# Optimization experiments

Hardware: AMD Instinct MI355X
Metric: run time of the kernel (lower is better)

The kernel has to match this reference:

```python
import jax, jax.numpy as jnp
import numpy as np

VOCAB = 100000
DIM = 128
B = 16384
CWIN = 10
K = 10
EPS = 1e-9


def setup_inputs() -> dict:
    key = jax.random.key(0)
    k1, k2, k3, k4, k5 = jax.random.split(key, 5)
    context = jax.random.randint(k1, (B, CWIN), 0, VOCAB)
    target = jax.random.randint(k2, (B,), 0, VOCAB)
    negatives = jax.random.randint(k3, (B, K), 0, VOCAB)
    in_emb = jax.random.normal(k4, (VOCAB, DIM), dtype=jnp.float32)
    out_emb = jax.random.normal(k5, (VOCAB, DIM), dtype=jnp.float32)
    return {"context": context, "target": target, "negatives": negatives,
            "in_emb": in_emb, "out_emb": out_emb}


def reference(context, target, negatives, in_emb, out_emb):
    # context: [B, C] int; target: [B] int; negatives: [B, K] int
    context_embed = in_emb[context]                      # [B, C, D]
    context_mean = jnp.mean(context_embed, axis=1)       # [B, D]
    target_embed = out_emb[target]                       # [B, D]
    neg_embed = out_emb[negatives]                       # [B, K, D]
    pos_score = jnp.sum(context_mean * target_embed, axis=1)          # [B]
    pos_loss = jnp.log(jax.nn.sigmoid(pos_score) + EPS)               # [B]
    neg_score = jnp.einsum('bkd,bd->bk', neg_embed, context_mean)     # [B, K]
    neg_loss = jnp.sum(jnp.log(jax.nn.sigmoid(-neg_score) + EPS), axis=1)  # [B]
    return -jnp.mean(pos_loss + neg_loss)
```

## Files before the change

kernel.cpp:

```cpp
#include <hip/hip_runtime.h>


#define VOCAB  100000
#define DIM    128
#define B_TOT  16384
#define CWIN   10
#define K_NEG  10
#define EPS_F  1e-9f

#define BPB    8
#define NBLK   (B_TOT / BPB)

__global__ __launch_bounds__(256, 8) void cbow_loss_kernel(
    const int*   __restrict__ context,
    const int*   __restrict__ target,
    const int*   __restrict__ negatives,
    const float* __restrict__ in_emb,
    const float* __restrict__ out_emb,
    float*       __restrict__ partials)
{
    const int tid  = threadIdx.x;
    const int halfId = tid >> 5;
    const int sub  = tid & 31;
    const int b    = blockIdx.x * BPB + halfId;

    const float4* in4  = (const float4*)in_emb;
    const float4* out4 = (const float4*)out_emb;

    float4 cm = make_float4(0.f, 0.f, 0.f, 0.f);
#pragma unroll
    for (int c = 0; c < CWIN; ++c) {
        const int idx = context[b * CWIN + c];
        const float4 v = in4[(size_t)idx * (DIM / 4) + sub];
        cm.x += v.x; cm.y += v.y; cm.z += v.z; cm.w += v.w;
    }
    cm.x *= (1.0f / CWIN); cm.y *= (1.0f / CWIN);
    cm.z *= (1.0f / CWIN); cm.w *= (1.0f / CWIN);

    float s[K_NEG + 1];
    {
        const int t = target[b];
        const float4 v = out4[(size_t)t * (DIM / 4) + sub];
        s[0] = cm.x * v.x + cm.y * v.y + cm.z * v.z + cm.w * v.w;
    }
#pragma unroll
    for (int k = 0; k < K_NEG; ++k) {
        const int idx = negatives[b * K_NEG + k];
        const float4 v = out4[(size_t)idx * (DIM / 4) + sub];
        s[k + 1] = cm.x * v.x + cm.y * v.y + cm.z * v.z + cm.w * v.w;
    }

#pragma unroll
    for (int j = 0; j <= K_NEG; ++j) {
        float x = s[j];
#pragma unroll
        for (int off = 16; off > 0; off >>= 1)
            x += __shfl_xor(x, off, 64);
        s[j] = x;
    }

    float l = __logf(1.0f / (1.0f + __expf(-s[0])) + EPS_F);
#pragma unroll
    for (int k = 1; k <= K_NEG; ++k)
        l += __logf(1.0f / (1.0f + __expf(s[k])) + EPS_F);

    __shared__ float part[BPB];
    if (sub == 0) part[halfId] = l;
    __syncthreads();
    if (tid == 0) {
        float t = 0.f;
#pragma unroll
        for (int i = 0; i < BPB; ++i) t += part[i];
        partials[blockIdx.x] = t;
    }
}

__global__ __launch_bounds__(256) void finalize_kernel(
    const float* __restrict__ partials,
    float*       __restrict__ out)
{
    const int tid  = threadIdx.x;
    const int lane = tid & 63;
    const int wave = tid >> 6;

    float x = 0.f;
#pragma unroll
    for (int j = 0; j < NBLK / 256; ++j)
        x += partials[tid + 256 * j];

#pragma unroll
    for (int off = 32; off > 0; off >>= 1)
        x += __shfl_xor(x, off, 64);

    __shared__ float part[4];
    if (lane == 0) part[wave] = x;
    __syncthreads();
    if (tid == 0)
        out[0] = -(part[0] + part[1] + part[2] + part[3]) * (1.0f / B_TOT);
}

extern "C" void kernel_launch(void* const* d_in, const int* in_sizes, int n_in,
                              void* d_out, int out_size, void* d_ws, size_t ws_size,
                              hipStream_t stream) {
    const int*   context   = (const int*)  d_in[0];
    const int*   target    = (const int*)  d_in[1];
    const int*   negatives = (const int*)  d_in[2];
    const float* in_emb    = (const float*)d_in[3];
    const float* out_emb   = (const float*)d_in[4];
    float*       out       = (float*)d_out;
    float*       partials  = (float*)d_ws;

    cbow_loss_kernel<<<NBLK, 256, 0, stream>>>(
        context, target, negatives, in_emb, out_emb, partials);
    finalize_kernel<<<1, 256, 0, stream>>>(partials, out);
}
```

Baseline: 134.1 us.

## Load indices once per lane and shuffle-broadcast, issue all row gathers upfront

Each lane of a 32-lane group now loads one of the context, negative or target indices, and the indices are broadcast by shuffle. This replaces the redundant per-thread index loads that sat in the dependency chain of every row gather. All 21 embedding rows are then gathered into registers before any arithmetic, so more loads are in flight at once. Occupancy bounds are relaxed to allow the extra registers. The in-block shared-memory reduction is dropped, so each batch element writes its own loss and the finalize kernel sums 16384 values instead of per-block partials. The index math is now 32-bit (idx<<5), which fits the vocab size.

```diff
diff --git a/kernel.cpp b/kernel.cpp
--- a/kernel.cpp
+++ b/kernel.cpp
@@ -11,44 +11,57 @@
 #define BPB    8
 #define NBLK   (B_TOT / BPB)
 
-__global__ __launch_bounds__(256, 8) void cbow_loss_kernel(
+__global__ __launch_bounds__(256, 4) void cbow_loss_kernel(
     const int*   __restrict__ context,
     const int*   __restrict__ target,
     const int*   __restrict__ negatives,
     const float* __restrict__ in_emb,
     const float* __restrict__ out_emb,
-    float*       __restrict__ partials)
+    float*       __restrict__ per_b)
 {
-    const int tid  = threadIdx.x;
+    const int tid    = threadIdx.x;
     const int halfId = tid >> 5;
-    const int sub  = tid & 31;
-    const int b    = blockIdx.x * BPB + halfId;
+    const int sub    = tid & 31;
+    const int b      = blockIdx.x * BPB + halfId;
 
     const float4* in4  = (const float4*)in_emb;
     const float4* out4 = (const float4*)out_emb;
 
+    int myIdx = 0;
+    {
+        const int* p  = target;
+        int        off = b;
+        if (sub < CWIN)                 { p = context;   off = b * CWIN + sub; }
+        else if (sub < 2 * CWIN)        { p = negatives; off = b * K_NEG + (sub - CWIN); }
+        if (sub <= 2 * CWIN) myIdx = p[off];
+    }
+
+    float4 cr[CWIN];
+#pragma unroll
+    for (int c = 0; c < CWIN; ++c) {
+        const int idx = __shfl(myIdx, c, 32);
+        cr[c] = in4[(idx << 5) + sub];
+    }
+    float4 ov[K_NEG + 1];
+#pragma unroll
+    for (int k = 0; k <= K_NEG; ++k) {
+        const int lanesrc = (k == 0) ? 2 * CWIN : (CWIN + k - 1);
+        const int idx = __shfl(myIdx, lanesrc, 32);
+        ov[k] = out4[(idx << 5) + sub];
+    }
+
     float4 cm = make_float4(0.f, 0.f, 0.f, 0.f);
 #pragma unroll
     for (int c = 0; c < CWIN; ++c) {
-        const int idx = context[b * CWIN + c];
-        const float4 v = in4[(size_t)idx * (DIM / 4) + sub];
-        cm.x += v.x; cm.y += v.y; cm.z += v.z; cm.w += v.w;
+        cm.x += cr[c].x; cm.y += cr[c].y; cm.z += cr[c].z; cm.w += cr[c].w;
     }
     cm.x *= (1.0f / CWIN); cm.y *= (1.0f / CWIN);
     cm.z *= (1.0f / CWIN); cm.w *= (1.0f / CWIN);
 
     float s[K_NEG + 1];
-    {
-        const int t = target[b];
-        const float4 v = out4[(size_t)t * (DIM / 4) + sub];
-        s[0] = cm.x * v.x + cm.y * v.y + cm.z * v.z + cm.w * v.w;
-    }
 #pragma unroll
-    for (int k = 0; k < K_NEG; ++k) {
-        const int idx = negatives[b * K_NEG + k];
-        const float4 v = out4[(size_t)idx * (DIM / 4) + sub];
-        s[k + 1] = cm.x * v.x + cm.y * v.y + cm.z * v.z + cm.w * v.w;
-    }
+    for (int k = 0; k <= K_NEG; ++k)
+        s[k] = cm.x * ov[k].x + cm.y * ov[k].y + cm.z * ov[k].z + cm.w * ov[k].w;
 
 #pragma unroll
     for (int j = 0; j <= K_NEG; ++j) {
@@ -64,19 +77,11 @@
     for (int k = 1; k <= K_NEG; ++k)
         l += __logf(1.0f / (1.0f + __expf(s[k])) + EPS_F);
 
-    __shared__ float part[BPB];
-    if (sub == 0) part[halfId] = l;
-    __syncthreads();
-    if (tid == 0) {
-        float t = 0.f;
-#pragma unroll
-        for (int i = 0; i < BPB; ++i) t += part[i];
-        partials[blockIdx.x] = t;
-    }
+    if (sub == 0) per_b[b] = l;
 }
 
 __global__ __launch_bounds__(256) void finalize_kernel(
-    const float* __restrict__ partials,
+    const float* __restrict__ per_b,
     float*       __restrict__ out)
 {
     const int tid  = threadIdx.x;
@@ -85,8 +90,8 @@
 
     float x = 0.f;
 #pragma unroll
-    for (int j = 0; j < NBLK / 256; ++j)
-        x += partials[tid + 256 * j];
+    for (int j = 0; j < B_TOT / 256; ++j)
+        x += per_b[tid + 256 * j];
 
 #pragma unroll
     for (int off = 32; off > 0; off >>= 1)
@@ -108,9 +113,9 @@
     const float* in_emb    = (const float*)d_in[3];
     const float* out_emb   = (const float*)d_in[4];
     float*       out       = (float*)d_out;
-    float*       partials  = (float*)d_ws;
+    float*       per_b     = (float*)d_ws;
 
     cbow_loss_kernel<<<NBLK, 256, 0, stream>>>(
-        context, target, negatives, in_emb, out_emb, partials);
-    finalize_kernel<<<1, 256, 0, stream>>>(partials, out);
+        context, target, negatives, in_emb, out_emb, per_b);
+    finalize_kernel<<<1, 256, 0, stream>>>(per_b, out);
 }
```

New measurement: 130.3 us. -2.8%, faster.
